# Performance work log

Measured on AMD Instinct MI355X. Metric: run time of the kernel, lower is better.

The kernel has to match this reference:

```python
import jax, jax.numpy as jnp
import numpy as np

D_MODEL = 2048
D_FF = 8192
EPS = 1e-5


def layernorm(x, g, b):
    m = x.mean(-1, keepdims=True)
    v = ((x - m) ** 2).mean(-1, keepdims=True)
    return (x - m) * jax.lax.rsqrt(v + EPS) * g + b


def rotate_half(x):
    return jnp.concatenate([-x[..., ::2], x[..., 1::2]], axis=-1)


def sinu_pos_emb(dim, length):
    inv_freq = 1.0 / 10000 ** (jnp.arange(0, dim, 2, dtype=jnp.float32) / dim)
    pos = jnp.arange(length, dtype=jnp.float32)
    sp = pos[:, None] * inv_freq[None, :]           # [S, dim/2]
    return jnp.concatenate([jnp.sin(sp), jnp.cos(sp)], axis=-1)  # [S, dim]


def setup_inputs() -> dict:
    key = jax.random.key(0)
    ks = jax.random.split(key, 10)
    d, f = D_MODEL, D_FF
    sc = 0.02
    return {
        "src":  jax.random.normal(ks[0], (4, 2048, d), jnp.float32),
        "Wqkv": jax.random.normal(ks[1], (3 * d, d), jnp.float32) * sc,
        "bqkv": jnp.zeros((3 * d,), jnp.float32),
        "Wo":   jax.random.normal(ks[2], (d, d), jnp.float32) * sc,
        "bo":   jnp.zeros((d,), jnp.float32),
        "W1":   jax.random.normal(ks[3], (f, d), jnp.float32) * sc,
        "b1":   jnp.zeros((f,), jnp.float32),
        "W2":   jax.random.normal(ks[4], (d, f), jnp.float32) * sc,
        "b2":   jnp.zeros((d,), jnp.float32),
        "g1":   jnp.ones((d,), jnp.float32),
        "be1":  jnp.zeros((d,), jnp.float32),
        "g2":   jnp.ones((d,), jnp.float32),
        "be2":  jnp.zeros((d,), jnp.float32),
    }


def reference(src, Wqkv, bqkv, Wo, bo, W1, b1, W2, b2, g1, be1, g2, be2):
    B, S, d = src.shape
    # norm1 (note: torch code reassigns src, so residuals use the normed value)
    src = layernorm(src, g1, be1)
    qkv = src @ Wqkv.T + bqkv                      # [B,S,3d]
    Q, K, V = qkv[..., :d], qkv[..., d:2 * d], qkv[..., 2 * d:]
    # rotary: cos/sin of the (sin,cos)-concatenated table, faithful to source
    emb = sinu_pos_emb(d, S)                       # [S,d]
    c, s = jnp.cos(emb), jnp.sin(emb)
    Q = Q * c + rotate_half(Q) * s
    K = K * c - rotate_half(K) * s
    # causal SDPA over full d_model (no head split in source)
    scale = 1.0 / jnp.sqrt(jnp.float32(d))
    scores = jnp.einsum('bqd,bkd->bqk', Q, K) * scale
    causal = jnp.tril(jnp.ones((S, S), bool))
    scores = jnp.where(causal, scores, jnp.float32(-1e30))
    P = jax.nn.softmax(scores, axis=-1)
    attn = jnp.einsum('bqk,bkd->bqd', P, V)
    src = src + attn @ Wo.T + bo
    # FFN block
    h = layernorm(src, g2, be2)
    h = jax.nn.relu(h @ W1.T + b1) @ W2.T + b2
    return src + h
```

## Files before the change

kernel.cpp:

```cpp
#include <hip/hip_runtime.h>
#include <cstdint>


typedef __attribute__((ext_vector_type(8))) short short8;
typedef __attribute__((ext_vector_type(4))) float floatx4;

#define PLANE 16777216L
#define SS    4194304L

__device__ __forceinline__ float bf2f(unsigned short u) {
    union { unsigned int i; float f; } v; v.i = ((unsigned int)u) << 16; return v.f;
}
__device__ __forceinline__ unsigned short f2bf(float f) {
    union { float f; unsigned int i; } v; v.f = f;
    unsigned int x = v.i;
    return (unsigned short)((x + 0x7FFFu + ((x >> 16) & 1u)) >> 16);
}
__device__ __forceinline__ uint4 pack8(float4 a, float4 b) {
    unsigned short o[8];
    o[0] = f2bf(a.x); o[1] = f2bf(a.y); o[2] = f2bf(a.z); o[3] = f2bf(a.w);
    o[4] = f2bf(b.x); o[5] = f2bf(b.y); o[6] = f2bf(b.z); o[7] = f2bf(b.w);
    return *(uint4*)o;
}
__device__ __forceinline__ void gl_lds16(const void* g, void* l) {
    __builtin_amdgcn_global_load_lds(
        (const __attribute__((address_space(1))) void*)g,
        (__attribute__((address_space(3))) void*)l, 16, 0, 0);
}

#define EM_QKV  0
#define EM_SC   1
#define EM_PV   2
#define EM_PROJ 3
#define EM_FFN1 4
#define EM_F2A  5

template<int EM>
__launch_bounds__(256, 2)
__global__ void gemm_bt(const unsigned short* __restrict__ A,
                        const unsigned short* __restrict__ B,
                        void* __restrict__ Cv, int N, int K,
                        const float* __restrict__ bias,
                        const unsigned short* __restrict__ resid16,
                        unsigned short* __restrict__ outQ,
                        unsigned short* __restrict__ outVt)
{
    constexpr int BM = 128, BN = 128, BK = 32;
    __shared__ __align__(16) unsigned short As[BM * BK];
    __shared__ __align__(16) unsigned short Bs[BN * BK];

    const int m0 = blockIdx.x * BM, n0 = blockIdx.y * BN;
    if (EM == EM_SC && n0 > m0 + (BM - 1)) return;

    int kmax = K;
    if (EM == EM_PV) { kmax = m0 + BM; if (kmax > K) kmax = K; }
    const int nsteps = kmax / BK;

    const int t = threadIdx.x;
    const int lane = t & 63, wave = t >> 6;
    const int q = lane >> 4, ln = lane & 15;
    const int wm = (wave >> 1) * 64, wn = (wave & 1) * 64;

    const int r0 = wave * 32;
    const int rA = r0 + (lane >> 2);
    const int cslot = lane & 3;
    const int cg0 = (cslot ^ (rA & 3)) * 8;
    const int cg1 = (cslot ^ ((rA + 16) & 3)) * 8;
    const unsigned short* Agp0 = A + (long)(m0 + rA) * K + cg0;
    const unsigned short* Agp1 = A + (long)(m0 + rA + 16) * K + cg1;
    const unsigned short* Bgp0 = B + (long)(n0 + rA) * K + cg0;
    const unsigned short* Bgp1 = B + (long)(n0 + rA + 16) * K + cg1;
    unsigned short* lA0 = &As[r0 * 32];
    unsigned short* lA1 = &As[(r0 + 16) * 32];
    unsigned short* lB0 = &Bs[r0 * 32];
    unsigned short* lB1 = &Bs[(r0 + 16) * 32];

    floatx4 acc[4][4];
#pragma unroll
    for (int i = 0; i < 4; ++i)
#pragma unroll
        for (int j = 0; j < 4; ++j) acc[i][j] = (floatx4){0.f, 0.f, 0.f, 0.f};

    for (int s = 0; s < nsteps; ++s) {
        const long off = (long)s * BK;
        __syncthreads();
        gl_lds16(Agp0 + off, lA0);
        gl_lds16(Agp1 + off, lA1);
        gl_lds16(Bgp0 + off, lB0);
        gl_lds16(Bgp1 + off, lB1);
        __syncthreads();
        short8 af[4], bfr[4];
#pragma unroll
        for (int i = 0; i < 4; ++i) {
            const int R = wm + 16 * i + ln;
            af[i] = *(const short8*)&As[R * 32 + ((q ^ (R & 3)) * 8)];
        }
#pragma unroll
        for (int j = 0; j < 4; ++j) {
            const int R = wn + 16 * j + ln;
            bfr[j] = *(const short8*)&Bs[R * 32 + ((q ^ (R & 3)) * 8)];
        }
#pragma unroll
        for (int i = 0; i < 4; ++i)
#pragma unroll
            for (int j = 0; j < 4; ++j)
                acc[i][j] = __builtin_amdgcn_mfma_f32_16x16x32_bf16(af[i], bfr[j], acc[i][j], 0, 0, 0);
    }

#pragma unroll
    for (int i = 0; i < 4; ++i) {
#pragma unroll
        for (int r = 0; r < 4; ++r) {
            const int row = m0 + wm + 16 * i + q * 4 + r;
#pragma unroll
            for (int j = 0; j < 4; ++j) {
                const int col = n0 + wn + 16 * j + ln;
                float v = acc[i][j][r];
                const long idx = (long)row * N + col;
                if constexpr (EM == EM_QKV) {
                    v += bias[col];
                    const unsigned short vb = f2bf(v);
                    const int p = col >> 11, c2 = col & 2047;
                    if (p == 0)      outQ[(long)row * 2048 + c2] = vb;
                    else if (p == 1) (outQ + PLANE)[(long)row * 2048 + c2] = vb;
                    else             outVt[(long)(row >> 11) * SS + (long)c2 * 2048 + (row & 2047)] = vb;
                } else if constexpr (EM == EM_SC) {
                    ((unsigned short*)Cv)[idx] = f2bf(v);
                } else if constexpr (EM == EM_PV) {
                    ((unsigned short*)Cv)[idx] = f2bf(v);
                } else if constexpr (EM == EM_PROJ) {
                    v += bias[col] + bf2f(resid16[idx]);
                    ((float*)Cv)[idx] = v;
                } else if constexpr (EM == EM_FFN1) {
                    v = fmaxf(v + bias[col], 0.f);
                    ((unsigned short*)Cv)[idx] = f2bf(v);
                } else {
                    ((float*)Cv)[idx] += v;
                }
            }
        }
    }
}

__launch_bounds__(256)
__global__ void cvt_rows(const float* __restrict__ src, unsigned short* __restrict__ dst, long srcld)
{
    const int row = blockIdx.x, t = threadIdx.x;
    const float* s = src + (long)row * srcld + t * 8;
    float4 a = *(const float4*)s;
    float4 b = *(const float4*)(s + 4);
    *(uint4*)(dst + (long)row * 2048 + t * 8) = pack8(a, b);
}

__launch_bounds__(256)
__global__ void layernorm_k(const float* __restrict__ X, unsigned short* __restrict__ Y,
                            const float* __restrict__ g, const float* __restrict__ be)
{
    const int row = blockIdx.x, t = threadIdx.x;
    const float* Xr = X + (long)row * 2048 + t * 8;
    float4 v0 = *(const float4*)Xr;
    float4 v1 = *(const float4*)(Xr + 4);
    float x[8] = {v0.x, v0.y, v0.z, v0.w, v1.x, v1.y, v1.z, v1.w};
    float s = 0.f, ss = 0.f;
#pragma unroll
    for (int k = 0; k < 8; ++k) { s += x[k]; ss += x[k] * x[k]; }
    for (int off = 32; off; off >>= 1) { s += __shfl_down(s, off, 64); ss += __shfl_down(ss, off, 64); }
    __shared__ float red[8];
    const int wave = t >> 6, lane = t & 63;
    if (lane == 0) { red[wave] = s; red[4 + wave] = ss; }
    __syncthreads();
    s  = red[0] + red[1] + red[2] + red[3];
    ss = red[4] + red[5] + red[6] + red[7];
    const float mean = s * (1.f / 2048.f);
    const float var  = ss * (1.f / 2048.f) - mean * mean;
    const float rstd = rsqrtf(var + 1e-5f);
    unsigned short o[8];
#pragma unroll
    for (int k = 0; k < 8; ++k) {
        const int col = t * 8 + k;
        o[k] = f2bf((x[k] - mean) * rstd * g[col] + be[col]);
    }
    *(uint4*)(Y + (long)row * 2048 + t * 8) = *(uint4*)o;
}

__launch_bounds__(256)
__global__ void rope_inplace(unsigned short* __restrict__ Q, unsigned short* __restrict__ K)
{
    __shared__ __align__(16) unsigned short rowbuf[2048];
    const int row = blockIdx.x;
    const int mtx = blockIdx.y;
    unsigned short* X = (mtx ? K : Q) + (long)row * 2048;
    const int t = threadIdx.x;
    *(uint4*)&rowbuf[t * 8] = *(const uint4*)(X + t * 8);
    __syncthreads();
    const int p = row & 2047;
    const float sgn = mtx ? -1.f : 1.f;
    unsigned short o[8];
#pragma unroll
    for (int e = 0; e < 8; ++e) {
        const int j = t * 8 + e;
        const int i = j & 1023;
        const float freq = __expf(-(float)i * (9.210340371976184f / 1024.0f));
        const float sp = (float)p * freq;
        const float emb = (j < 1024) ? sinf(sp) : cosf(sp);
        float se, ce;
        sincosf(emb, &se, &ce);
        const int pj = (j < 1024) ? (2 * j) : (2 * j - 2047);
        float xp = bf2f(rowbuf[pj]);
        if (j < 1024) xp = -xp;
        o[e] = f2bf(bf2f(rowbuf[j]) * ce + sgn * xp * se);
    }
    *(uint4*)(X + t * 8) = *(uint4*)o;
}

__launch_bounds__(256)
__global__ void softmax_causal(unsigned short* __restrict__ S)
{
    const int qq = blockIdx.x;
    const int L = qq + 1;
    unsigned short* srow = S + (long)qq * 2048;
    const int t = threadIdx.x;
    const float scale = 0.022097086912079608f;
    float vals[8];
    float m = -1e30f;
#pragma unroll
    for (int u = 0; u < 8; ++u) {
        const int i2 = t + 256 * u;
        vals[u] = (i2 < L) ? bf2f(srow[i2]) * scale : -1e30f;
        m = fmaxf(m, vals[u]);
    }
    for (int off = 32; off; off >>= 1) m = fmaxf(m, __shfl_down(m, off, 64));
    __shared__ float red[8];
    const int wave = t >> 6, lane = t & 63;
    if (lane == 0) red[wave] = m;
    __syncthreads();
    m = fmaxf(fmaxf(red[0], red[1]), fmaxf(red[2], red[3]));
    float sum = 0.f;
#pragma unroll
    for (int u = 0; u < 8; ++u) {
        float e = __expf(vals[u] - m);
        e = (t + 256 * u < L) ? e : 0.f;
        vals[u] = e; sum += e;
    }
    for (int off = 32; off; off >>= 1) sum += __shfl_down(sum, off, 64);
    if (lane == 0) red[4 + wave] = sum;
    __syncthreads();
    sum = red[4] + red[5] + red[6] + red[7];
    const float inv = 1.0f / sum;
#pragma unroll
    for (int u = 0; u < 8; ++u) srow[t + 256 * u] = f2bf(vals[u] * inv);
}

__launch_bounds__(256)
__global__ void final_add(float* __restrict__ io, const float* __restrict__ b2)
{
    const int row = blockIdx.x, t = threadIdx.x;
    const long base = (long)row * 2048 + t * 8;
    float4 a0 = *(const float4*)(io + base);
    float4 a1 = *(const float4*)(io + base + 4);
    float4 c0 = *(const float4*)(b2 + t * 8);
    float4 c1 = *(const float4*)(b2 + t * 8 + 4);
    a0.x += c0.x; a0.y += c0.y; a0.z += c0.z; a0.w += c0.w;
    a1.x += c1.x; a1.y += c1.y; a1.z += c1.z; a1.w += c1.w;
    *(float4*)(io + base) = a0;
    *(float4*)(io + base + 4) = a1;
}

extern "C" void kernel_launch(void* const* d_in, const int* in_sizes, int n_in,
                              void* d_out, int out_size, void* d_ws, size_t ws_size,
                              hipStream_t stream)
{
    const float* src  = (const float*)d_in[0];
    const float* Wqkv = (const float*)d_in[1];
    const float* bqkv = (const float*)d_in[2];
    const float* Wo   = (const float*)d_in[3];
    const float* bo   = (const float*)d_in[4];
    const float* W1   = (const float*)d_in[5];
    const float* b1   = (const float*)d_in[6];
    const float* W2   = (const float*)d_in[7];
    const float* b2   = (const float*)d_in[8];
    const float* g1   = (const float*)d_in[9];
    const float* be1  = (const float*)d_in[10];
    const float* g2   = (const float*)d_in[11];
    const float* be2  = (const float*)d_in[12];

    char* ws = (char*)d_ws;
    const long MB = 1LL << 20;
    unsigned short* x1    = (unsigned short*)ws;
    unsigned short* Vt    = (unsigned short*)(ws + 32 * MB);
    unsigned short* Wqbf  = (unsigned short*)(ws + 64 * MB);
    unsigned short* attn  = (unsigned short*)(ws + 64 * MB);
    unsigned short* scP   = (unsigned short*)(ws + 96 * MB);
    unsigned short* Wobf  = (unsigned short*)(ws + 96 * MB);
    unsigned short* W1c   = (unsigned short*)(ws + 96 * MB);
    unsigned short* W2c   = (unsigned short*)(ws + 104 * MB);
    unsigned short* h2    = x1;
    unsigned short* f1    = Vt;

    unsigned short* Q    = (unsigned short*)d_out;
    float*          src2 = (float*)d_out;
    float*          out  = (float*)d_out;

    const dim3 blk(256);

    cvt_rows<<<6144, blk, 0, stream>>>(Wqkv, Wqbf, 2048);
    layernorm_k<<<8192, blk, 0, stream>>>(src, x1, g1, be1);
    gemm_bt<EM_QKV><<<dim3(64, 48), blk, 0, stream>>>(
        x1, Wqbf, nullptr, 6144, 2048, bqkv, nullptr, Q, Vt);
    rope_inplace<<<dim3(8192, 2), blk, 0, stream>>>(Q, Q + PLANE);

    for (int b = 0; b < 4; ++b) {
        gemm_bt<EM_SC><<<dim3(16, 16), blk, 0, stream>>>(
            Q + b * SS, Q + PLANE + b * SS, scP, 2048, 2048, nullptr, nullptr, nullptr, nullptr);
        softmax_causal<<<2048, blk, 0, stream>>>(scP);
        gemm_bt<EM_PV><<<dim3(16, 16), blk, 0, stream>>>(
            scP, Vt + b * SS, attn + b * SS, 2048, 2048, nullptr, nullptr, nullptr, nullptr);
    }

    cvt_rows<<<2048, blk, 0, stream>>>(Wo, Wobf, 2048);
    gemm_bt<EM_PROJ><<<dim3(64, 16), blk, 0, stream>>>(
        attn, Wobf, src2, 2048, 2048, bo, x1, nullptr, nullptr);
    layernorm_k<<<8192, blk, 0, stream>>>(src2, h2, g2, be2);

    for (int c = 0; c < 4; ++c) {
        cvt_rows<<<2048, blk, 0, stream>>>(W1 + (long)c * 2048 * 2048, W1c, 2048);
        cvt_rows<<<2048, blk, 0, stream>>>(W2 + (long)c * 2048, W2c, 8192);
        gemm_bt<EM_FFN1><<<dim3(64, 16), blk, 0, stream>>>(
            h2, W1c, f1, 2048, 2048, b1 + c * 2048, nullptr, nullptr, nullptr);
        gemm_bt<EM_F2A><<<dim3(64, 16), blk, 0, stream>>>(
            f1, W2c, src2, 2048, 2048, nullptr, nullptr, nullptr, nullptr);
    }
    final_add<<<8192, blk, 0, stream>>>(out, b2);
}
```

Before: 1.669 ms.

## Add 256x256-tile 512-thread pipelined GEMM for QKV, projection and FFN

Introduces a new gemm256 kernel with 256x256 output tiles, 8 waves, double-buffered LDS loads via direct global-to-LDS copies, interleaved MFMA and staging with barriers and s_setprio. QKV, output projection and both FFN GEMMs switch to it, while the score and PV GEMMs keep the old 128-tile kernel. Larger tiles raise arithmetic intensity and cut global traffic, at the cost of fewer blocks (e.g. 256 for the 2048x2048 GEMMs) and heavy register and LDS use (64KB LDS per block).

```diff
diff --git a/kernel.cpp b/kernel.cpp
--- a/kernel.cpp
+++ b/kernel.cpp
@@ -117,6 +117,183 @@
                 const int col = n0 + wn + 16 * j + ln;
                 float v = acc[i][j][r];
                 const long idx = (long)row * N + col;
+                if constexpr (EM == EM_SC) {
+                    ((unsigned short*)Cv)[idx] = f2bf(v);
+                } else if constexpr (EM == EM_PV) {
+                    ((unsigned short*)Cv)[idx] = f2bf(v);
+                }
+            }
+        }
+    }
+}
+
+#define BAR()    __builtin_amdgcn_s_barrier()
+#define LGKM0()  asm volatile("s_waitcnt lgkmcnt(0)" ::: "memory")
+#define VMCNT(n) asm volatile("s_waitcnt vmcnt(" #n ")" ::: "memory")
+
+template<int EM>
+__launch_bounds__(512, 2)
+__global__ void gemm256(const unsigned short* __restrict__ A,
+                        const unsigned short* __restrict__ B,
+                        void* __restrict__ Cv, int N, int K,
+                        const float* __restrict__ bias,
+                        const unsigned short* __restrict__ resid16,
+                        unsigned short* __restrict__ outQ,
+                        unsigned short* __restrict__ outVt)
+{
+    __shared__ __align__(16) unsigned short As[2][16384];
+    __shared__ __align__(16) unsigned short Bs[2][16384];
+
+    const int m0 = blockIdx.x * 256, n0 = blockIdx.y * 256;
+    const int t = threadIdx.x;
+    const int lane = t & 63, wave = t >> 6;
+    const int q = lane >> 4, ln = lane & 15;
+    const int wm = wave >> 2, wn = wave & 3;
+
+    const int jrow = lane >> 3;
+    const int csrc = ((lane & 7) ^ jrow) * 8;
+    const unsigned short* Ag = A + (long)(m0 + wave * 16 + jrow) * K + csrc;
+    const unsigned short* Bg = B + (long)(n0 + wave * 16 + jrow) * K + csrc;
+    const int ldsSlice = wave * 1024;
+
+    const int aBase = (wm * 128 + ln) * 64;
+    const int bBase = (wn * 64 + ln) * 64;
+    const int c0 = ((0 + q) ^ (ln & 7)) * 8;
+    const int c1 = ((4 + q) ^ (ln & 7)) * 8;
+
+    floatx4 acc[8][4];
+#pragma unroll
+    for (int i = 0; i < 8; ++i)
+#pragma unroll
+        for (int j = 0; j < 4; ++j) acc[i][j] = (floatx4){0.f, 0.f, 0.f, 0.f};
+
+    short8 a[4][2];
+    short8 b[2][2][2];
+
+#define STAGE_A(buf, kt, h) do { \
+    const unsigned short* _g = Ag + (long)((h) * 128) * K + ((long)(kt) << 6); \
+    gl_lds16(_g,          &As[buf][(h) * 8192 + ldsSlice]); \
+    gl_lds16(_g + 8L * K, &As[buf][(h) * 8192 + ldsSlice + 512]); \
+} while (0)
+#define STAGE_B(buf, kt, h) do { \
+    const unsigned short* _g = Bg + (long)((h) * 128) * K + ((long)(kt) << 6); \
+    gl_lds16(_g,          &Bs[buf][(h) * 8192 + ldsSlice]); \
+    gl_lds16(_g + 8L * K, &Bs[buf][(h) * 8192 + ldsSlice + 512]); \
+} while (0)
+#define RD_A(sel, mg) { \
+    _Pragma("unroll") \
+    for (int i = 0; i < 4; ++i) { \
+        a[i][0] = *(const short8*)&As[sel][aBase + ((mg) * 64 + 16 * i) * 64 + c0]; \
+        a[i][1] = *(const short8*)&As[sel][aBase + ((mg) * 64 + 16 * i) * 64 + c1]; \
+    } }
+#define RD_B(sel, ng) { \
+    _Pragma("unroll") \
+    for (int j = 0; j < 2; ++j) { \
+        b[ng][j][0] = *(const short8*)&Bs[sel][bBase + ((ng) * 32 + 16 * j) * 64 + c0]; \
+        b[ng][j][1] = *(const short8*)&Bs[sel][bBase + ((ng) * 32 + 16 * j) * 64 + c1]; \
+    } }
+#define MM(mg, ng) { \
+    _Pragma("unroll") \
+    for (int i = 0; i < 4; ++i) \
+    _Pragma("unroll") \
+    for (int j = 0; j < 2; ++j) { \
+        acc[(mg)*4+i][(ng)*2+j] = __builtin_amdgcn_mfma_f32_16x16x32_bf16( \
+            a[i][0], b[ng][j][0], acc[(mg)*4+i][(ng)*2+j], 0, 0, 0); \
+        acc[(mg)*4+i][(ng)*2+j] = __builtin_amdgcn_mfma_f32_16x16x32_bf16( \
+            a[i][1], b[ng][j][1], acc[(mg)*4+i][(ng)*2+j], 0, 0, 0); \
+    } }
+
+    const int nIter = K >> 7;
+
+    STAGE_A(0, 0, 0); STAGE_A(0, 0, 1);
+    STAGE_B(0, 0, 0); STAGE_B(0, 0, 1);
+    STAGE_B(1, 1, 0); STAGE_B(1, 1, 1);
+    VMCNT(4); BAR();
+
+    for (int it = 0; it < nIter - 1; ++it) {
+        const int k1 = 2 * it + 1, ke = 2 * it + 2, ko = 2 * it + 3;
+        RD_A(0, 0); RD_B(0, 0);
+        STAGE_A(1, k1, 0);
+        BAR(); LGKM0();
+        __builtin_amdgcn_s_setprio(1); MM(0, 0); __builtin_amdgcn_s_setprio(0);
+        BAR();
+        RD_B(0, 1);
+        STAGE_A(1, k1, 1);
+        BAR(); LGKM0();
+        __builtin_amdgcn_s_setprio(1); MM(0, 1); __builtin_amdgcn_s_setprio(0);
+        BAR();
+        RD_A(0, 1);
+        STAGE_B(0, ke, 0);
+        BAR(); LGKM0();
+        __builtin_amdgcn_s_setprio(1); MM(1, 0); __builtin_amdgcn_s_setprio(0);
+        BAR();
+        STAGE_B(0, ke, 1);
+        BAR();
+        __builtin_amdgcn_s_setprio(1); MM(1, 1); __builtin_amdgcn_s_setprio(0);
+        VMCNT(4); BAR();
+        RD_A(1, 0); RD_B(1, 0);
+        STAGE_A(0, ke, 0);
+        BAR(); LGKM0();
+        __builtin_amdgcn_s_setprio(1); MM(0, 0); __builtin_amdgcn_s_setprio(0);
+        BAR();
+        RD_B(1, 1);
+        STAGE_A(0, ke, 1);
+        BAR(); LGKM0();
+        __builtin_amdgcn_s_setprio(1); MM(0, 1); __builtin_amdgcn_s_setprio(0);
+        BAR();
+        RD_A(1, 1);
+        STAGE_B(1, ko, 0);
+        BAR(); LGKM0();
+        __builtin_amdgcn_s_setprio(1); MM(1, 0); __builtin_amdgcn_s_setprio(0);
+        BAR();
+        STAGE_B(1, ko, 1);
+        BAR();
+        __builtin_amdgcn_s_setprio(1); MM(1, 1); __builtin_amdgcn_s_setprio(0);
+        VMCNT(4); BAR();
+    }
+
+    {
+        const int k1 = 2 * nIter - 1;
+        RD_A(0, 0); RD_B(0, 0);
+        STAGE_A(1, k1, 0);
+        BAR(); LGKM0();
+        __builtin_amdgcn_s_setprio(1); MM(0, 0); __builtin_amdgcn_s_setprio(0);
+        BAR();
+        RD_B(0, 1);
+        STAGE_A(1, k1, 1);
+        BAR(); LGKM0();
+        __builtin_amdgcn_s_setprio(1); MM(0, 1); __builtin_amdgcn_s_setprio(0);
+        BAR();
+        RD_A(0, 1);
+        BAR(); LGKM0();
+        __builtin_amdgcn_s_setprio(1); MM(1, 0); __builtin_amdgcn_s_setprio(0);
+        BAR();
+        __builtin_amdgcn_s_setprio(1); MM(1, 1); __builtin_amdgcn_s_setprio(0);
+        VMCNT(0); BAR();
+        RD_A(1, 0); RD_B(1, 0);
+        MM(0, 0);
+        RD_B(1, 1);
+        MM(0, 1);
+        RD_A(1, 1);
+        MM(1, 0); MM(1, 1);
+    }
+
+#undef STAGE_A
+#undef STAGE_B
+#undef RD_A
+#undef RD_B
+#undef MM
+
+#pragma unroll
+    for (int i = 0; i < 8; ++i) {
+#pragma unroll
+        for (int r = 0; r < 4; ++r) {
+            const int row = m0 + wm * 128 + 16 * i + q * 4 + r;
+#pragma unroll
+            for (int j = 0; j < 4; ++j) {
+                const int col = n0 + wn * 64 + 16 * j + ln;
+                float v = acc[i][j][r];
+                const long idx = (long)row * N + col;
                 if constexpr (EM == EM_QKV) {
                     v += bias[col];
                     const unsigned short vb = f2bf(v);
@@ -124,10 +301,6 @@
                     if (p == 0)      outQ[(long)row * 2048 + c2] = vb;
                     else if (p == 1) (outQ + PLANE)[(long)row * 2048 + c2] = vb;
                     else             outVt[(long)(row >> 11) * SS + (long)c2 * 2048 + (row & 2047)] = vb;
-                } else if constexpr (EM == EM_SC) {
-                    ((unsigned short*)Cv)[idx] = f2bf(v);
-                } else if constexpr (EM == EM_PV) {
-                    ((unsigned short*)Cv)[idx] = f2bf(v);
                 } else if constexpr (EM == EM_PROJ) {
                     v += bias[col] + bf2f(resid16[idx]);
                     ((float*)Cv)[idx] = v;
@@ -302,10 +475,11 @@
     float*          out  = (float*)d_out;
 
     const dim3 blk(256);
+    const dim3 blk512(512);
 
     cvt_rows<<<6144, blk, 0, stream>>>(Wqkv, Wqbf, 2048);
     layernorm_k<<<8192, blk, 0, stream>>>(src, x1, g1, be1);
-    gemm_bt<EM_QKV><<<dim3(64, 48), blk, 0, stream>>>(
+    gemm256<EM_QKV><<<dim3(32, 24), blk512, 0, stream>>>(
         x1, Wqbf, nullptr, 6144, 2048, bqkv, nullptr, Q, Vt);
     rope_inplace<<<dim3(8192, 2), blk, 0, stream>>>(Q, Q + PLANE);
 
@@ -318,16 +492,16 @@
     }
 
     cvt_rows<<<2048, blk, 0, stream>>>(Wo, Wobf, 2048);
-    gemm_bt<EM_PROJ><<<dim3(64, 16), blk, 0, stream>>>(
+    gemm256<EM_PROJ><<<dim3(32, 8), blk512, 0, stream>>>(
         attn, Wobf, src2, 2048, 2048, bo, x1, nullptr, nullptr);
     layernorm_k<<<8192, blk, 0, stream>>>(src2, h2, g2, be2);
 
     for (int c = 0; c < 4; ++c) {
         cvt_rows<<<2048, blk, 0, stream>>>(W1 + (long)c * 2048 * 2048, W1c, 2048);
         cvt_rows<<<2048, blk, 0, stream>>>(W2 + (long)c * 2048, W2c, 8192);
-        gemm_bt<EM_FFN1><<<dim3(64, 16), blk, 0, stream>>>(
+        gemm256<EM_FFN1><<<dim3(32, 8), blk512, 0, stream>>>(
             h2, W1c, f1, 2048, 2048, b1 + c * 2048, nullptr, nullptr, nullptr);
-        gemm_bt<EM_F2A><<<dim3(64, 16), blk, 0, stream>>>(
+        gemm256<EM_F2A><<<dim3(32, 8), blk512, 0, stream>>>(
             f1, W2c, src2, 2048, 2048, nullptr, nullptr, nullptr, nullptr);
     }
     final_add<<<8192, blk, 0, stream>>>(out, b2);
```

Measured after the change: 1.527 ms. 8.5% less time.
